# Performance work log

Hardware: AMD Instinct MI355X
Metric: run time of the kernel (lower is better)

Reference implementation:

```python
import jax, jax.numpy as jnp
import numpy as np

N, D = 262144, 128

def setup_inputs() -> dict:
    key = jax.random.key(0)
    x = jax.random.normal(key, (N, D), dtype=jnp.float32)
    return {"x": x, "k": 102, "n_iters": 10}

def reference(x, k, n_iters):
    # x.view(x.size(0), -1): flatten trailing dims
    x = x.reshape(x.shape[0], -1)
    # deterministic init: first k points as centroids
    c = x[:k]  # [k, D]
    x_sq = jnp.sum(x * x, axis=1, keepdims=True)  # [N, 1]
    labels = jnp.zeros((x.shape[0],), dtype=jnp.int32)
    for _ in range(n_iters):
        # squared Euclidean distances [N, k] (cdist^2, argmin-equivalent to cdist)
        d2 = x_sq - 2.0 * (x @ c.T) + jnp.sum(c * c, axis=1)
        labels = jnp.argmin(d2, axis=1).astype(jnp.int32)
        # scatter-mean centroid update
        sums = jax.ops.segment_sum(x, labels, num_segments=k)          # [k, D]
        counts = jax.ops.segment_sum(jnp.ones((x.shape[0],), x.dtype), labels, num_segments=k)  # [k]
        new_c = sums / jnp.maximum(counts, 1.0)[:, None]
        c = jnp.where(counts[:, None] > 0, new_c, c)  # keep old centroid for empty clusters
    return labels
```

## Files before the change

kernel.cpp:

```cpp
#include <hip/hip_runtime.h>

#define NPTS   262144
#define DIM    128
#define DIM4   32
#define KC     102
#define NITERS 10
#define NBLK_H 512
#define CHK    512


#define WS_CA    0
#define WS_CB    53248
#define WS_CSQ   106496
#define WS_CNT   107520
#define WS_CBASE 108544
#define WS_H     109568
#define WS_OFFS  318464
#define WS_PT    527360
#define WS_NEED  1575936

__global__ void k_fill(int* __restrict__ p, int n, int v)
{
    const int i = blockIdx.x * 256 + threadIdx.x;
    if (i < n) p[i] = v;
}

__device__ __forceinline__ float np_sumsq128(const float* a)
{
#pragma clang fp contract(off)
    float r[8];
    #pragma unroll
    for (int t = 0; t < 8; ++t) { const float v = a[t]; r[t] = v * v; }
    #pragma unroll
    for (int i = 8; i < 128; i += 8) {
        #pragma unroll
        for (int t = 0; t < 8; ++t) { const float v = a[i + t]; r[t] += v * v; }
    }
    return ((r[0] + r[1]) + (r[2] + r[3])) + ((r[4] + r[5]) + (r[6] + r[7]));
}

__device__ __forceinline__ float xr_get(const float4* xr, int i)
{
    const float4 v = xr[i >> 2];
    const int c = i & 3;
    return c == 0 ? v.x : c == 1 ? v.y : c == 2 ? v.z : v.w;
}

__device__ __forceinline__ float np_sumsq128_reg(const float4* xr)
{
#pragma clang fp contract(off)
    float r[8];
    #pragma unroll
    for (int t = 0; t < 8; ++t) { const float v = xr_get(xr, t); r[t] = v * v; }
    #pragma unroll
    for (int i = 8; i < 128; i += 8) {
        #pragma unroll
        for (int t = 0; t < 8; ++t) { const float v = xr_get(xr, i + t); r[t] += v * v; }
    }
    return ((r[0] + r[1]) + (r[2] + r[3])) + ((r[4] + r[5]) + (r[6] + r[7]));
}

__global__ __launch_bounds__(128)
void k_initc(const float* __restrict__ x, float* __restrict__ c, float* __restrict__ csq)
{
    __shared__ float row[DIM];
    const int j = blockIdx.x, d = threadIdx.x;
    const float v = x[(size_t)j * DIM + d];
    c[j * DIM + d] = v;
    row[d] = v;
    __syncthreads();
    if (d == 0) csq[j] = np_sumsq128(row);
}

__global__ __launch_bounds__(256, 2)
void k_assign(const float* __restrict__ x, const float* __restrict__ c,
              const float* __restrict__ csq, int* __restrict__ labels)
{
    __shared__ float4 cl[KC * DIM4];
    __shared__ float  sj[KC];
    for (int i = threadIdx.x; i < KC * DIM4; i += 256)
        cl[i] = reinterpret_cast<const float4*>(c)[i];
    for (int i = threadIdx.x; i < KC; i += 256) sj[i] = csq[i];
    __syncthreads();

    const int p = blockIdx.x * 256 + threadIdx.x;
    const float4* xp = reinterpret_cast<const float4*>(x) + (size_t)p * DIM4;
    float4 xr[DIM4];
    #pragma unroll
    for (int q = 0; q < DIM4; ++q) xr[q] = xp[q];

    float best1 = 3.4e38f, best2 = 3.4e38f;
    int bi = 0;
    for (int j = 0; j < KC; ++j) {
        const float4* cj = &cl[j * DIM4];
        float a0 = 0.f, a1 = 0.f, a2 = 0.f, a3 = 0.f;
        #pragma unroll
        for (int q = 0; q < DIM4; ++q) {
            const float4 cv = cj[q];
            a0 = __builtin_fmaf(xr[q].x, cv.x, a0);
            a1 = __builtin_fmaf(xr[q].y, cv.y, a1);
            a2 = __builtin_fmaf(xr[q].z, cv.z, a2);
            a3 = __builtin_fmaf(xr[q].w, cv.w, a3);
        }
        const float F = sj[j] - 2.0f * ((a0 + a1) + (a2 + a3));
        if (F < best1)      { best2 = best1; best1 = F; bi = j; }
        else if (F < best2) { best2 = F; }
    }

    int lab = bi;
    if (best2 - best1 < 0.02f) {
        const float Tp  = np_sumsq128_reg(xr);
        const float win = best1 + 0.02f;
        float bestE = 3.4e38f;
        int bj = bi;
        for (int j = 0; j < KC; ++j) {
            const float4* cj = &cl[j * DIM4];
            float a0 = 0.f, a1 = 0.f, a2 = 0.f, a3 = 0.f;
            #pragma unroll
            for (int q = 0; q < DIM4; ++q) {
                const float4 cv = cj[q];
                a0 = __builtin_fmaf(xr[q].x, cv.x, a0);
                a1 = __builtin_fmaf(xr[q].y, cv.y, a1);
                a2 = __builtin_fmaf(xr[q].z, cv.z, a2);
                a3 = __builtin_fmaf(xr[q].w, cv.w, a3);
            }
            const float F = sj[j] - 2.0f * ((a0 + a1) + (a2 + a3));
            if (F <= win) {
                float t0 = 0.f, t1 = 0.f;
                #pragma unroll
                for (int q = 0; q < DIM4; ++q) {
                    const float4 cv = cj[q];
                    t0 = __builtin_fmaf(xr[q].x, cv.x, t0);
                    t1 = __builtin_fmaf(xr[q].y, cv.y, t1);
                    t0 = __builtin_fmaf(xr[q].z, cv.z, t0);
                    t1 = __builtin_fmaf(xr[q].w, cv.w, t1);
                }
                float E;
                {
#pragma clang fp contract(off)
                    const float D = t0 + t1;
                    const float u = Tp - 2.0f * D;
                    E = u + sj[j];
                }
                if (E < bestE) { bestE = E; bj = j; }
            }
        }
        lab = bj;
    }
    labels[p] = lab;
}

__global__ __launch_bounds__(256)
void k_hist(const int* __restrict__ labels, int* __restrict__ H)
{
    __shared__ int h[KC];
    for (int i = threadIdx.x; i < KC; i += 256) h[i] = 0;
    __syncthreads();
    const int b = blockIdx.x;
    #pragma unroll
    for (int u = 0; u < 2; ++u)
        atomicAdd(&h[labels[b * CHK + u * 256 + threadIdx.x]], 1);
    __syncthreads();
    for (int i = threadIdx.x; i < KC; i += 256) H[i * NBLK_H + b] = h[i];
}

__global__ __launch_bounds__(128)
void k_scan(const int* __restrict__ H, int* __restrict__ OFFS,
            int* __restrict__ counts, int* __restrict__ cbase)
{
    __shared__ int tot[KC];
    const int j = threadIdx.x;
    if (j < KC) {
        int run = 0;
        for (int b = 0; b < NBLK_H; ++b) { OFFS[j * NBLK_H + b] = run; run += H[j * NBLK_H + b]; }
        tot[j] = run;
    }
    __syncthreads();
    if (j == 0) {
        int base = 0;
        for (int jj = 0; jj < KC; ++jj) { cbase[jj] = base; counts[jj] = tot[jj]; base += tot[jj]; }
    }
}

__global__ __launch_bounds__(64)
void k_scatter(const int* __restrict__ labels, const int* __restrict__ OFFS,
               const int* __restrict__ cbase, int* __restrict__ ptidx)
{
    __shared__ int lab[CHK];
    __shared__ int lrank[KC];
    __shared__ int soff[KC];
    const int b = blockIdx.x;
    for (int i = threadIdx.x; i < CHK; i += 64) lab[i] = labels[b * CHK + i];
    for (int i = threadIdx.x; i < KC; i += 64) { lrank[i] = 0; soff[i] = cbase[i] + OFFS[i * NBLK_H + b]; }
    __syncthreads();
    if (threadIdx.x == 0) {
        for (int i = 0; i < CHK; ++i) {
            const int l = lab[i];
            ptidx[soff[l] + lrank[l]++] = b * CHK + i;
        }
    }
}

__global__ __launch_bounds__(128)
void k_update(const float* __restrict__ x, const int* __restrict__ ptidx,
              const int* __restrict__ counts, const int* __restrict__ cbase,
              const float* __restrict__ cold, float* __restrict__ cnew,
              float* __restrict__ csq)
{
    __shared__ int   spt[CHK];
    __shared__ float row[DIM];
    const int j = blockIdx.x, d = threadIdx.x;
    const int n = counts[j], base = cbase[j];

    float s = 0.f;
    for (int c0 = 0; c0 < n; c0 += CHK) {
        const int m = min(CHK, n - c0);
        __syncthreads();
        for (int i = d; i < m; i += 128) spt[i] = ptidx[base + c0 + i];
        __syncthreads();
        const int nfull = m & ~31;
        float vA[32], vB[32];
        if (nfull >= 32) {
            #pragma unroll
            for (int u = 0; u < 32; ++u) vA[u] = x[(size_t)spt[u] * DIM + d];
        }
        int q = 0;
        while (q * 32 < nfull) {
            if ((q + 1) * 32 < nfull) {
                #pragma unroll
                for (int u = 0; u < 32; ++u) vB[u] = x[(size_t)spt[(q+1)*32+u] * DIM + d];
            }
            {
#pragma clang fp contract(off)
                #pragma unroll
                for (int u = 0; u < 32; ++u) s += vA[u];
            }
            ++q;
            if (q * 32 >= nfull) break;
            if ((q + 1) * 32 < nfull) {
                #pragma unroll
                for (int u = 0; u < 32; ++u) vA[u] = x[(size_t)spt[(q+1)*32+u] * DIM + d];
            }
            {
#pragma clang fp contract(off)
                #pragma unroll
                for (int u = 0; u < 32; ++u) s += vB[u];
            }
            ++q;
        }
        {
#pragma clang fp contract(off)
            for (int t = nfull; t < m; ++t) s += x[(size_t)spt[t] * DIM + d];
        }
    }

    const float v = (n > 0) ? (s / fmaxf((float)n, 1.0f)) : cold[j * DIM + d];
    cnew[j * DIM + d] = v;
    row[d] = v;
    __syncthreads();
    if (d == 0) csq[j] = np_sumsq128(row);
}

extern "C" void kernel_launch(void* const* d_in, const int* in_sizes, int n_in,
                              void* d_out, int out_size, void* d_ws, size_t ws_size,
                              hipStream_t stream)
{
    int* labels = (int*)d_out;

    const float* x = nullptr;
    for (int i = 0; i < n_in; ++i)
        if (in_sizes[i] == NPTS * DIM) { x = (const float*)d_in[i]; break; }
    if (!x)                        { k_fill<<<(NPTS+255)/256, 256, 0, stream>>>(labels, NPTS, 2000); return; }
    if (ws_size < (size_t)WS_NEED) { k_fill<<<(NPTS+255)/256, 256, 0, stream>>>(labels, NPTS, 3000); return; }

    char* w = (char*)d_ws;
    float* c_a    = (float*)(w + WS_CA);
    float* c_b    = (float*)(w + WS_CB);
    float* csq    = (float*)(w + WS_CSQ);
    int*   counts = (int*)  (w + WS_CNT);
    int*   cbase  = (int*)  (w + WS_CBASE);
    int*   H      = (int*)  (w + WS_H);
    int*   OFFS   = (int*)  (w + WS_OFFS);
    int*   ptidx  = (int*)  (w + WS_PT);

    k_initc<<<KC, 128, 0, stream>>>(x, c_a, csq);

    float* c_cur = c_a;
    float* c_nxt = c_b;
    for (int it = 0; it < NITERS; ++it) {
        k_assign<<<NPTS / 256, 256, 0, stream>>>(x, c_cur, csq, labels);
        if (it < NITERS - 1) {
            k_hist   <<<NBLK_H, 256, 0, stream>>>(labels, H);
            k_scan   <<<1, 128, 0, stream>>>(H, OFFS, counts, cbase);
            k_scatter<<<NBLK_H, 64, 0, stream>>>(labels, OFFS, cbase, ptidx);
            k_update <<<KC, 128, 0, stream>>>(x, ptidx, counts, cbase, c_cur, c_nxt, csq);
            float* tmp = c_cur; c_cur = c_nxt; c_nxt = tmp;
        }
    }
}
```

Before: 6.120 ms.

## Gather points into cluster-sorted buffer before centroid update

Adds a full-grid gather kernel that copies each point's row into a cluster-contiguous workspace buffer using float4 accesses. The per-centroid update kernel then streams contiguous rows through double-buffered shared memory instead of doing scattered per-element indexed loads. This targets the poorly parallel, latency-bound gather in the 102-block update kernel, at the cost of an extra full pass writing and reading a 128 MB buffer per iteration. It only runs when the workspace is large enough, and the fallback path's manual register prefetching is simplified to a plain loop.

```diff
diff --git a/kernel.cpp b/kernel.cpp
--- a/kernel.cpp
+++ b/kernel.cpp
@@ -17,7 +17,9 @@
 #define WS_H     109568
 #define WS_OFFS  318464
 #define WS_PT    527360
-#define WS_NEED  1575936
+#define WS_SMALL 1575936
+#define WS_XG    2097152
+#define WS_BIG   (WS_XG + (size_t)NPTS * DIM * 4)
 
 __global__ void k_fill(int* __restrict__ p, int n, int v)
 {
@@ -201,6 +203,59 @@
     }
 }
 
+__global__ __launch_bounds__(256)
+void k_gather(const float* __restrict__ x, const int* __restrict__ ptidx,
+              float* __restrict__ xg)
+{
+    const int i = blockIdx.x * 8 + (threadIdx.x >> 5);
+    const int q = threadIdx.x & 31;
+    const int p = ptidx[i];
+    reinterpret_cast<float4*>(xg)[(size_t)i * DIM4 + q] =
+        reinterpret_cast<const float4*>(x)[(size_t)p * DIM4 + q];
+}
+
+__global__ __launch_bounds__(128)
+void k_update_lin(const float* __restrict__ xg, const int* __restrict__ counts,
+                  const int* __restrict__ cbase, const float* __restrict__ cold,
+                  float* __restrict__ cnew, float* __restrict__ csq)
+{
+    __shared__ float buf[2][32][DIM];
+    __shared__ float row[DIM];
+    const int j = blockIdx.x, d = threadIdx.x;
+    const int n = counts[j];
+    const size_t rowbase = (size_t)cbase[j];
+
+    const int nc = (n + 31) >> 5;
+
+    auto stage = [&](int b, int r0, int cnt) {
+        const float4* src = reinterpret_cast<const float4*>(xg) + (rowbase + r0) * DIM4;
+        float4* dst = reinterpret_cast<float4*>(&buf[b][0][0]);
+        for (int i = d; i < cnt * DIM4; i += 128) dst[i] = src[i];
+    };
+
+    float s = 0.f;
+    if (n > 0) {
+        stage(0, 0, min(32, n));
+        __syncthreads();
+        for (int c = 0; c < nc; ++c) {
+            const int m = min(32, n - c * 32);
+            if (c + 1 < nc) stage((c + 1) & 1, (c + 1) * 32, min(32, n - (c + 1) * 32));
+            {
+#pragma clang fp contract(off)
+                const float* col = &buf[c & 1][0][d];
+                for (int r = 0; r < m; ++r) s += col[(size_t)r * DIM];
+            }
+            __syncthreads();
+        }
+    }
+
+    const float v = (n > 0) ? (s / fmaxf((float)n, 1.0f)) : cold[j * DIM + d];
+    cnew[j * DIM + d] = v;
+    row[d] = v;
+    __syncthreads();
+    if (d == 0) csq[j] = np_sumsq128(row);
+}
+
 __global__ __launch_bounds__(128)
 void k_update(const float* __restrict__ x, const int* __restrict__ ptidx,
               const int* __restrict__ counts, const int* __restrict__ cbase,
@@ -218,39 +273,9 @@
         __syncthreads();
         for (int i = d; i < m; i += 128) spt[i] = ptidx[base + c0 + i];
         __syncthreads();
-        const int nfull = m & ~31;
-        float vA[32], vB[32];
-        if (nfull >= 32) {
-            #pragma unroll
-            for (int u = 0; u < 32; ++u) vA[u] = x[(size_t)spt[u] * DIM + d];
-        }
-        int q = 0;
-        while (q * 32 < nfull) {
-            if ((q + 1) * 32 < nfull) {
-                #pragma unroll
-                for (int u = 0; u < 32; ++u) vB[u] = x[(size_t)spt[(q+1)*32+u] * DIM + d];
-            }
-            {
-#pragma clang fp contract(off)
-                #pragma unroll
-                for (int u = 0; u < 32; ++u) s += vA[u];
-            }
-            ++q;
-            if (q * 32 >= nfull) break;
-            if ((q + 1) * 32 < nfull) {
-                #pragma unroll
-                for (int u = 0; u < 32; ++u) vA[u] = x[(size_t)spt[(q+1)*32+u] * DIM + d];
-            }
-            {
-#pragma clang fp contract(off)
-                #pragma unroll
-                for (int u = 0; u < 32; ++u) s += vB[u];
-            }
-            ++q;
-        }
         {
 #pragma clang fp contract(off)
-            for (int t = nfull; t < m; ++t) s += x[(size_t)spt[t] * DIM + d];
+            for (int t = 0; t < m; ++t) s += x[(size_t)spt[t] * DIM + d];
         }
     }
 
@@ -270,8 +295,10 @@
     const float* x = nullptr;
     for (int i = 0; i < n_in; ++i)
         if (in_sizes[i] == NPTS * DIM) { x = (const float*)d_in[i]; break; }
-    if (!x)                        { k_fill<<<(NPTS+255)/256, 256, 0, stream>>>(labels, NPTS, 2000); return; }
-    if (ws_size < (size_t)WS_NEED) { k_fill<<<(NPTS+255)/256, 256, 0, stream>>>(labels, NPTS, 3000); return; }
+    if (!x)                         { k_fill<<<(NPTS+255)/256, 256, 0, stream>>>(labels, NPTS, 2000); return; }
+    if (ws_size < (size_t)WS_SMALL) { k_fill<<<(NPTS+255)/256, 256, 0, stream>>>(labels, NPTS, 3000); return; }
+
+    const bool big = ws_size >= (size_t)WS_BIG;
 
     char* w = (char*)d_ws;
     float* c_a    = (float*)(w + WS_CA);
@@ -282,6 +309,7 @@
     int*   H      = (int*)  (w + WS_H);
     int*   OFFS   = (int*)  (w + WS_OFFS);
     int*   ptidx  = (int*)  (w + WS_PT);
+    float* xg     = (float*)(w + WS_XG);
 
     k_initc<<<KC, 128, 0, stream>>>(x, c_a, csq);
 
@@ -293,7 +321,12 @@
             k_hist   <<<NBLK_H, 256, 0, stream>>>(labels, H);
             k_scan   <<<1, 128, 0, stream>>>(H, OFFS, counts, cbase);
             k_scatter<<<NBLK_H, 64, 0, stream>>>(labels, OFFS, cbase, ptidx);
-            k_update <<<KC, 128, 0, stream>>>(x, ptidx, counts, cbase, c_cur, c_nxt, csq);
+            if (big) {
+                k_gather    <<<NPTS / 8, 256, 0, stream>>>(x, ptidx, xg);
+                k_update_lin<<<KC, 128, 0, stream>>>(xg, counts, cbase, c_cur, c_nxt, csq);
+            } else {
+                k_update    <<<KC, 128, 0, stream>>>(x, ptidx, counts, cbase, c_cur, c_nxt, csq);
+            }
             float* tmp = c_cur; c_cur = c_nxt; c_nxt = tmp;
         }
     }
```

Result: slower. 10.21 ms (+66.8%).
